# Performance work log

Measured on AMD Instinct MI355X. Metric: run time of the kernel, lower is better.

## Reference

```python
import jax, jax.numpy as jnp
import numpy as np

B, D1, D2, D3 = 4, 64, 64, 64
CIN, COUT = 32, 32
M1, M2, M3 = 8, 8, 8


def setup_inputs() -> dict:
    key = jax.random.key(0)
    k1, k2, k3 = jax.random.split(key, 3)
    x = jax.random.normal(k1, (B, D1, D2, D3, CIN), dtype=jnp.float32)
    # scale ~ random_normal initializer (stddev 0.05 default in keras)
    w_real = jax.random.normal(k2, (CIN, COUT, M1, M2, M3), dtype=jnp.float32) * 0.05
    w_imag = jax.random.normal(k3, (CIN, COUT, M1, M2, M3), dtype=jnp.float32) * 0.05
    return {"x": x, "w_real": w_real, "w_imag": w_imag}


def reference(x, w_real, w_imag):
    # tf.signal.fft3d transforms the innermost 3 dims of [B,D1,D2,D3,C]
    x_ft = jnp.fft.fftn(x.astype(jnp.complex64), axes=(2, 3, 4))
    # low-mode truncation over axes 1,2,3 (as in the original code)
    x_low = x_ft[:, :M1, :M2, :M3, :]                       # [B,M1,M2,M3,CIN]
    w = (w_real + 1j * w_imag).astype(jnp.complex64)         # [CIN,COUT,M1,M2,M3]
    x_low = jnp.transpose(x_low, (0, 4, 1, 2, 3))            # [B,CIN,M1,M2,M3]
    # Faithful to original: i,j of weights are summed out, k is matched.
    out_low = jnp.einsum('bcmnk,coijk->bomnk', x_low, w)     # [B,COUT,M1,M2,M3]
    out_low = jnp.transpose(out_low, (0, 2, 3, 4, 1))        # [B,M1,M2,M3,COUT]
    # zero-padded spectrum (replaces the wasteful tensor_scatter_nd_update)
    out_ft = jnp.zeros((B, D1, D2, D3, COUT), dtype=jnp.complex64)
    out_ft = out_ft.at[:, :M1, :M2, :M3, :].set(out_low)
    y = jnp.fft.ifftn(out_ft, axes=(2, 3, 4))
    return jnp.real(y).astype(jnp.float32)
```

## Files before the change

### kernel.cpp

```cpp
#include <hip/hip_runtime.h>


#define PI2F 6.28318530717958647692f

__device__ __forceinline__ void twmul_acc(float vx, float vy, int t, int N,
                                          float sign, float& re, float& im) {
    float ang = sign * (PI2F / (float)N) * (float)t;
    float s, c;
    __sincosf(ang, &s, &c);
    re += vx * c - vy * s;
    im += vx * s + vy * c;
}

__global__ void k_weff(const float* __restrict__ wr, const float* __restrict__ wi,
                       float2* __restrict__ Weff) {
    int t = blockIdx.x * 256 + threadIdx.x;
    if (t >= 8192) return;
    int base = (t >> 3) * 512 + (t & 7);
    float sr = 0.f, si = 0.f;
    #pragma unroll 8
    for (int ij = 0; ij < 64; ++ij) { sr += wr[base + ij * 8]; si += wi[base + ij * 8]; }
    Weff[t] = make_float2(sr, si);
}

__global__ void k_dft_d2(const float* __restrict__ x, float2* __restrict__ S1) {
    int t = blockIdx.x * 256 + threadIdx.x;
    int c  = t & 31;
    int d3 = (t >> 5) & 63;
    int f2 = (t >> 11) & 7;
    int d1 = (t >> 14) & 7;
    int b  = t >> 17;
    const float* xp = x + (size_t)b * 8388608 + (size_t)d1 * 131072 + d3 * 32 + c;
    float re = 0.f, im = 0.f;
    for (int d2 = 0; d2 < 64; ++d2) {
        float v = xp[d2 * 2048];
        twmul_acc(v, 0.f, (f2 * d2) & 63, 64, -1.f, re, im);
    }
    S1[t] = make_float2(re, im);
}

__global__ void k_dft_d3(const float2* __restrict__ S1, float2* __restrict__ S2) {
    int t = blockIdx.x * 256 + threadIdx.x;
    int c  = t & 31;
    int f3 = (t >> 5) & 7;
    int hi = t >> 8;
    const float2* p = S1 + (size_t)hi * 2048 + c;
    float re = 0.f, im = 0.f;
    for (int d3 = 0; d3 < 64; ++d3) {
        float2 v = p[d3 * 32];
        twmul_acc(v.x, v.y, (f3 * d3) & 63, 64, -1.f, re, im);
    }
    S2[t] = make_float2(re, im);
}

__global__ void k_dft_c(const float2* __restrict__ S2, float2* __restrict__ S3) {
    int t = blockIdx.x * 256 + threadIdx.x;
    int fc = t & 31;
    int base = t & ~31;
    float re = 0.f, im = 0.f;
    for (int c = 0; c < 32; ++c) {
        float2 v = S2[base + c];
        twmul_acc(v.x, v.y, (fc * c) & 31, 32, -1.f, re, im);
    }
    S3[t] = make_float2(re, im);
}

__global__ void k_mix(const float2* __restrict__ S3, const float2* __restrict__ Weff,
                      float2* __restrict__ S4) {
    int t = blockIdx.x * 256 + threadIdx.x;
    int o  = t & 31;
    int f3 = (t >> 5) & 7;
    int base = t & ~31;
    float re = 0.f, im = 0.f;
    for (int fc = 0; fc < 32; ++fc) {
        float2 a = S3[base + fc];
        float2 w = Weff[(fc * 32 + o) * 8 + f3];
        re += a.x * w.x - a.y * w.y;
        im += a.x * w.y + a.y * w.x;
    }
    S4[t] = make_float2(re, im);
}

__global__ void k_idft_c(const float2* __restrict__ S4, float2* __restrict__ S5) {
    int t = blockIdx.x * 256 + threadIdx.x;
    int co = t & 31;
    int base = t & ~31;
    float re = 0.f, im = 0.f;
    for (int o = 0; o < 32; ++o) {
        float2 v = S4[base + o];
        twmul_acc(v.x, v.y, (o * co) & 31, 32, 1.f, re, im);
    }
    S5[t] = make_float2(re, im);
}

__global__ void k_idft_d3(const float2* __restrict__ S5, float2* __restrict__ S6) {
    int t = blockIdx.x * 256 + threadIdx.x;
    int co = t & 31;
    int d3 = (t >> 5) & 63;
    int bd1f2 = t >> 11;
    const float2* p = S5 + bd1f2 * 256 + co;
    float re = 0.f, im = 0.f;
    #pragma unroll
    for (int f3 = 0; f3 < 8; ++f3) {
        float2 v = p[f3 * 32];
        twmul_acc(v.x, v.y, (f3 * d3) & 63, 64, 1.f, re, im);
    }
    S6[t] = make_float2(re, im);
}

__global__ void k_final(const float2* __restrict__ S6, float* __restrict__ out) {
    int t4 = blockIdx.x * 256 + threadIdx.x;
    int u = t4 << 2;
    int co = u & 31;
    int d3 = (u >> 5) & 63;
    int d2 = (u >> 11) & 63;
    int d1 = (u >> 17) & 63;
    int b  = u >> 23;
    float4 r;
    if (d1 >= 8) {
        r = make_float4(0.f, 0.f, 0.f, 0.f);
    } else {
        const float2* q = S6 + (size_t)(b * 8 + d1) * 16384 + d3 * 32 + co;
        float a0 = 0.f, a1 = 0.f, a2 = 0.f, a3 = 0.f;
        #pragma unroll
        for (int f2 = 0; f2 < 8; ++f2) {
            float ang = (PI2F / 64.f) * (float)((f2 * d2) & 63);
            float s, c;
            __sincosf(ang, &s, &c);
            float2 v0 = q[f2 * 2048 + 0];
            float2 v1 = q[f2 * 2048 + 1];
            float2 v2 = q[f2 * 2048 + 2];
            float2 v3 = q[f2 * 2048 + 3];
            a0 += v0.x * c - v0.y * s;
            a1 += v1.x * c - v1.y * s;
            a2 += v2.x * c - v2.y * s;
            a3 += v3.x * c - v3.y * s;
        }
        const float sc = 1.f / 131072.f;
        r = make_float4(a0 * sc, a1 * sc, a2 * sc, a3 * sc);
    }
    ((float4*)out)[t4] = r;
}

extern "C" void kernel_launch(void* const* d_in, const int* in_sizes, int n_in,
                              void* d_out, int out_size, void* d_ws, size_t ws_size,
                              hipStream_t stream) {
    const float* x  = (const float*)d_in[0];
    const float* wr = (const float*)d_in[1];
    const float* wi = (const float*)d_in[2];
    float* out = (float*)d_out;

    float2* Weff = (float2*)d_ws;
    float2* S1 = Weff + 8192;
    float2* S2 = S1 + 524288;
    float2* S3 = S2 + 65536;
    float2* S4 = S3 + 65536;
    float2* S5 = S4 + 65536;
    float2* S6 = S5 + 65536;

    k_weff   <<<32,    256, 0, stream>>>(wr, wi, Weff);
    k_dft_d2 <<<2048,  256, 0, stream>>>(x, S1);
    k_dft_d3 <<<256,   256, 0, stream>>>(S1, S2);
    k_dft_c  <<<256,   256, 0, stream>>>(S2, S3);
    k_mix    <<<256,   256, 0, stream>>>(S3, Weff, S4);
    k_idft_c <<<256,   256, 0, stream>>>(S4, S5);
    k_idft_d3<<<2048,  256, 0, stream>>>(S5, S6);
    k_final  <<<32768, 256, 0, stream>>>(S6, out);
}
```

Baseline: 265.5 us.

## Fold channel DFTs into weight matrix and fuse middle spectral stages

```diff
diff --git a/kernel.cpp b/kernel.cpp
--- a/kernel.cpp
+++ b/kernel.cpp
@@ -3,19 +3,13 @@
 
 #define PI2F 6.28318530717958647692f
 
-__device__ __forceinline__ void twmul_acc(float vx, float vy, int t, int N,
-                                          float sign, float& re, float& im) {
-    float ang = sign * (PI2F / (float)N) * (float)t;
-    float s, c;
-    __sincosf(ang, &s, &c);
-    re += vx * c - vy * s;
-    im += vx * s + vy * c;
+__device__ __forceinline__ float2 cmul(float2 a, float2 b) {
+    return make_float2(a.x * b.x - a.y * b.y, a.x * b.y + a.y * b.x);
 }
 
 __global__ void k_weff(const float* __restrict__ wr, const float* __restrict__ wi,
                        float2* __restrict__ Weff) {
     int t = blockIdx.x * 256 + threadIdx.x;
-    if (t >= 8192) return;
     int base = (t >> 3) * 512 + (t & 7);
     float sr = 0.f, si = 0.f;
     #pragma unroll 8
@@ -23,89 +17,132 @@
     Weff[t] = make_float2(sr, si);
 }
 
+__global__ void k_T(const float2* __restrict__ Weff, float2* __restrict__ T) {
+    __shared__ float2 tw32[32];
+    __shared__ float2 A[256];
+    int t = threadIdx.x;
+    int c = blockIdx.x;
+    if (t < 32) {
+        float s, co_;
+        __sincosf((PI2F / 32.f) * (float)t, &s, &co_);
+        tw32[t] = make_float2(co_, s);
+    }
+    __syncthreads();
+    {
+        float2 acc = make_float2(0.f, 0.f);
+        for (int fc = 0; fc < 32; ++fc) {
+            float2 v = Weff[fc * 256 + t];
+            float2 e = tw32[(fc * c) & 31];
+            acc.x += v.x * e.x + v.y * e.y;
+            acc.y += v.y * e.x - v.x * e.y;
+        }
+        A[t] = acc;
+    }
+    __syncthreads();
+    {
+        int f3 = t >> 5, co = t & 31;
+        float2 acc = make_float2(0.f, 0.f);
+        for (int o = 0; o < 32; ++o) {
+            float2 v = A[o * 8 + f3];
+            float2 e = tw32[(o * co) & 31];
+            acc.x += v.x * e.x - v.y * e.y;
+            acc.y += v.x * e.y + v.y * e.x;
+        }
+        T[c * 256 + t] = acc;
+    }
+}
+
 __global__ void k_dft_d2(const float* __restrict__ x, float2* __restrict__ S1) {
     int t = blockIdx.x * 256 + threadIdx.x;
-    int c  = t & 31;
-    int d3 = (t >> 5) & 63;
-    int f2 = (t >> 11) & 7;
-    int d1 = (t >> 14) & 7;
-    int b  = t >> 17;
-    const float* xp = x + (size_t)b * 8388608 + (size_t)d1 * 131072 + d3 * 32 + c;
-    float re = 0.f, im = 0.f;
+    int c4 = t & 7;
+    int d3 = (t >> 3) & 63;
+    int f2 = (t >> 9) & 7;
+    int d1 = (t >> 12) & 7;
+    int b  = t >> 15;
+    const float4* xp = (const float4*)(x + (size_t)b * 8388608 + (size_t)d1 * 131072
+                                         + d3 * 32 + c4 * 4);
+    float s, c;
+    __sincosf((PI2F / 64.f) * (float)f2, &s, &c);
+    float2 step = make_float2(c, -s);
+    float2 w = make_float2(1.f, 0.f);
+    float2 a0 = {0,0}, a1 = {0,0}, a2 = {0,0}, a3 = {0,0};
     for (int d2 = 0; d2 < 64; ++d2) {
-        float v = xp[d2 * 2048];
-        twmul_acc(v, 0.f, (f2 * d2) & 63, 64, -1.f, re, im);
-    }
-    S1[t] = make_float2(re, im);
-}
-
-__global__ void k_dft_d3(const float2* __restrict__ S1, float2* __restrict__ S2) {
-    int t = blockIdx.x * 256 + threadIdx.x;
-    int c  = t & 31;
-    int f3 = (t >> 5) & 7;
-    int hi = t >> 8;
-    const float2* p = S1 + (size_t)hi * 2048 + c;
-    float re = 0.f, im = 0.f;
-    for (int d3 = 0; d3 < 64; ++d3) {
-        float2 v = p[d3 * 32];
-        twmul_acc(v.x, v.y, (f3 * d3) & 63, 64, -1.f, re, im);
-    }
-    S2[t] = make_float2(re, im);
-}
-
-__global__ void k_dft_c(const float2* __restrict__ S2, float2* __restrict__ S3) {
-    int t = blockIdx.x * 256 + threadIdx.x;
-    int fc = t & 31;
-    int base = t & ~31;
-    float re = 0.f, im = 0.f;
-    for (int c = 0; c < 32; ++c) {
-        float2 v = S2[base + c];
-        twmul_acc(v.x, v.y, (fc * c) & 31, 32, -1.f, re, im);
-    }
-    S3[t] = make_float2(re, im);
-}
-
-__global__ void k_mix(const float2* __restrict__ S3, const float2* __restrict__ Weff,
-                      float2* __restrict__ S4) {
-    int t = blockIdx.x * 256 + threadIdx.x;
-    int o  = t & 31;
-    int f3 = (t >> 5) & 7;
-    int base = t & ~31;
-    float re = 0.f, im = 0.f;
-    for (int fc = 0; fc < 32; ++fc) {
-        float2 a = S3[base + fc];
-        float2 w = Weff[(fc * 32 + o) * 8 + f3];
-        re += a.x * w.x - a.y * w.y;
-        im += a.x * w.y + a.y * w.x;
-    }
-    S4[t] = make_float2(re, im);
-}
-
-__global__ void k_idft_c(const float2* __restrict__ S4, float2* __restrict__ S5) {
-    int t = blockIdx.x * 256 + threadIdx.x;
-    int co = t & 31;
-    int base = t & ~31;
-    float re = 0.f, im = 0.f;
-    for (int o = 0; o < 32; ++o) {
-        float2 v = S4[base + o];
-        twmul_acc(v.x, v.y, (o * co) & 31, 32, 1.f, re, im);
-    }
-    S5[t] = make_float2(re, im);
-}
-
-__global__ void k_idft_d3(const float2* __restrict__ S5, float2* __restrict__ S6) {
-    int t = blockIdx.x * 256 + threadIdx.x;
-    int co = t & 31;
-    int d3 = (t >> 5) & 63;
-    int bd1f2 = t >> 11;
-    const float2* p = S5 + bd1f2 * 256 + co;
-    float re = 0.f, im = 0.f;
-    #pragma unroll
-    for (int f3 = 0; f3 < 8; ++f3) {
-        float2 v = p[f3 * 32];
-        twmul_acc(v.x, v.y, (f3 * d3) & 63, 64, 1.f, re, im);
-    }
-    S6[t] = make_float2(re, im);
+        float4 v = xp[d2 * 512];
+        a0.x += v.x * w.x; a0.y += v.x * w.y;
+        a1.x += v.y * w.x; a1.y += v.y * w.y;
+        a2.x += v.z * w.x; a2.y += v.z * w.y;
+        a3.x += v.w * w.x; a3.y += v.w * w.y;
+        w = cmul(w, step);
+    }
+    float2* sp = S1 + (size_t)(t >> 9) * 2048 + d3 * 32 + c4 * 4;
+    ((float4*)sp)[0] = make_float4(a0.x, a0.y, a1.x, a1.y);
+    ((float4*)sp)[1] = make_float4(a2.x, a2.y, a3.x, a3.y);
+}
+
+__global__ void k_mid(const float2* __restrict__ S1, const float2* __restrict__ T,
+                      float2* __restrict__ S6) {
+    __shared__ float2 lin[2048];
+    __shared__ float2 ls2[256];
+    __shared__ float2 ls5[256];
+    __shared__ float2 tw64[64];
+    int t = threadIdx.x;
+    int gid = blockIdx.x;
+    {
+        const float4* src = (const float4*)(S1 + (size_t)gid * 2048);
+        float4* dst = (float4*)lin;
+        #pragma unroll
+        for (int j = 0; j < 4; ++j) dst[t + j * 256] = src[t + j * 256];
+    }
+    if (t < 64) {
+        float s, c;
+        __sincosf((PI2F / 64.f) * (float)t, &s, &c);
+        tw64[t] = make_float2(c, s);
+    }
+    __syncthreads();
+    {
+        int f3 = t >> 5, c = t & 31;
+        float2 e = tw64[f3];
+        float2 step = make_float2(e.x, -e.y);
+        float2 w = make_float2(1.f, 0.f);
+        float2 acc = make_float2(0.f, 0.f);
+        for (int d3 = 0; d3 < 64; ++d3) {
+            float2 v = lin[d3 * 32 + c];
+            acc.x += v.x * w.x - v.y * w.y;
+            acc.y += v.x * w.y + v.y * w.x;
+            w = cmul(w, step);
+        }
+        ls2[f3 * 32 + c] = acc;
+    }
+    __syncthreads();
+    {
+        int f3 = t >> 5;
+        float2 acc = make_float2(0.f, 0.f);
+        for (int c = 0; c < 32; ++c) {
+            float2 a = ls2[f3 * 32 + (c)];
+            float2 w = T[c * 256 + t];
+            acc.x += a.x * w.x - a.y * w.y;
+            acc.y += a.x * w.y + a.y * w.x;
+        }
+        ls5[t] = acc;
+    }
+    __syncthreads();
+    {
+        int co = t & 31, d3r = t >> 5;
+        float2* outp = S6 + (size_t)gid * 2048;
+        #pragma unroll
+        for (int j = 0; j < 8; ++j) {
+            int d3 = d3r + 8 * j;
+            float2 acc = make_float2(0.f, 0.f);
+            #pragma unroll
+            for (int f3 = 0; f3 < 8; ++f3) {
+                float2 v = ls5[f3 * 32 + co];
+                float2 e = tw64[(f3 * d3) & 63];
+                acc.x += v.x * e.x - v.y * e.y;
+                acc.y += v.x * e.y + v.y * e.x;
+            }
+            outp[d3 * 32 + co] = acc;
+        }
+    }
 }
 
 __global__ void k_final(const float2* __restrict__ S6, float* __restrict__ out) {
@@ -151,19 +188,13 @@
     float* out = (float*)d_out;
 
     float2* Weff = (float2*)d_ws;
-    float2* S1 = Weff + 8192;
-    float2* S2 = S1 + 524288;
-    float2* S3 = S2 + 65536;
-    float2* S4 = S3 + 65536;
-    float2* S5 = S4 + 65536;
-    float2* S6 = S5 + 65536;
-
-    k_weff   <<<32,    256, 0, stream>>>(wr, wi, Weff);
-    k_dft_d2 <<<2048,  256, 0, stream>>>(x, S1);
-    k_dft_d3 <<<256,   256, 0, stream>>>(S1, S2);
-    k_dft_c  <<<256,   256, 0, stream>>>(S2, S3);
-    k_mix    <<<256,   256, 0, stream>>>(S3, Weff, S4);
-    k_idft_c <<<256,   256, 0, stream>>>(S4, S5);
-    k_idft_d3<<<2048,  256, 0, stream>>>(S5, S6);
-    k_final  <<<32768, 256, 0, stream>>>(S6, out);
-}
+    float2* T    = Weff + 8192;
+    float2* S1   = T + 8192;
+    float2* S6   = S1 + 524288;
+
+    k_weff  <<<32,    256, 0, stream>>>(wr, wi, Weff);
+    k_T     <<<32,    256, 0, stream>>>(Weff, T);
+    k_dft_d2<<<512,   256, 0, stream>>>(x, S1);
+    k_mid   <<<256,   256, 0, stream>>>(S1, T, S6);
+    k_final <<<32768, 256, 0, stream>>>(S6, out);
+}
```

New measurement: 238.3 us. 1.11x faster.
